# Kernel optimization log

Measured on AMD Instinct MI355X. Metric: run time of the kernel, lower is better.

Reference implementation:

```python
import jax, jax.numpy as jnp
import numpy as np
from functools import partial

K = 10
ALPHA = 0.1
N_NODES = 100000
N_EDGES = 1600000
IN_C, HID_C, OUT_C = 512, 256, 64


def setup_inputs() -> dict:
    key = jax.random.key(0)
    k1, k2, k3, k4, k5 = jax.random.split(key, 5)
    x = jax.random.normal(k1, (N_NODES, IN_C), dtype=jnp.float32)
    edge_index = jax.random.randint(k2, (2, N_EDGES), 0, N_NODES, dtype=jnp.int64)
    # Linear params (torch Linear: y = x @ W.T + b), Kaiming-ish scale
    w1 = jax.random.normal(k3, (HID_C, IN_C), dtype=jnp.float32) / np.sqrt(IN_C)
    b1 = jnp.zeros((HID_C,), dtype=jnp.float32)
    w2 = jax.random.normal(k4, (OUT_C, HID_C), dtype=jnp.float32) / np.sqrt(HID_C)
    b2 = jnp.zeros((OUT_C,), dtype=jnp.float32)
    return {"x": x, "edge_index": edge_index, "w1": w1, "b1": b1, "w2": w2, "b2": b2}


def _gcn_norm(edge_index, num_nodes):
    # add self-loops, symmetric normalization: norm_e = d[src]^-1/2 * d[dst]^-1/2
    loops = jnp.arange(num_nodes, dtype=edge_index.dtype)
    src = jnp.concatenate([edge_index[0], loops])
    dst = jnp.concatenate([edge_index[1], loops])
    ones = jnp.ones_like(dst, dtype=jnp.float32)
    deg = jax.ops.segment_sum(ones, dst, num_segments=num_nodes)
    dinv = jnp.where(deg > 0, jax.lax.rsqrt(deg), 0.0)
    norm = dinv[src] * dinv[dst]
    return src, dst, norm


def reference(x, edge_index, w1, b1, w2, b2):
    # inference mode: dropout = identity
    h = jax.nn.relu(x @ w1.T + b1)
    h = h @ w2.T + b2  # [N, OUT_C]
    n = x.shape[0]
    src, dst, norm = _gcn_norm(edge_index, n)
    h0 = h

    def step(hcur, _):
        msg = hcur[src] * norm[:, None]                      # gather [E+N, C]
        agg = jax.ops.segment_sum(msg, dst, num_segments=n)  # scatter-add [N, C]
        return (1.0 - ALPHA) * agg + ALPHA * h0, None

    h, _ = jax.lax.scan(step, h, None, length=K)
    return h
```

## Files before the change

### kernel.cpp

```cpp
#include <hip/hip_runtime.h>
#include <hip/hip_bf16.h>

#define N_NODES 100000
#define N_EDGES 1600000
#define IN_C 512
#define HID_C 256
#define OUT_C 64
#define K_ITERS 10
#define ALPHA 0.1f

typedef float f32x4 __attribute__((ext_vector_type(4)));
typedef _Float16 f16;
typedef _Float16 f16x4 __attribute__((ext_vector_type(4)));
typedef _Float16 f16x8 __attribute__((ext_vector_type(8)));

#define MFMA16(a, b, c) __builtin_amdgcn_mfma_f32_16x16x32_f16((a), (b), (c), 0, 0, 0)

__device__ __forceinline__ void gload16(const void* g, void* l) {
    __builtin_amdgcn_global_load_lds(
        (const __attribute__((address_space(1))) unsigned int*)g,
        (__attribute__((address_space(3))) unsigned int*)l, 16, 0, 0);
}

__global__ void k_count(const int* __restrict__ ei, int* __restrict__ cnt, int E) {
    int e = blockIdx.x * blockDim.x + threadIdx.x;
    if (e < E) atomicAdd(&cnt[ei[E + e]], 1);
}

__global__ void k_dinv(const int* __restrict__ cnt, float* __restrict__ dinv, int n) {
    int i = blockIdx.x * blockDim.x + threadIdx.x;
    if (i < n) dinv[i] = rsqrtf((float)cnt[i] + 1.0f);
}

#define SCB 1024
__global__ __launch_bounds__(256) void k_scan1(const int* __restrict__ cnt,
                                               int* __restrict__ bsum, int n) {
    __shared__ int s[256];
    int b = blockIdx.x, t = threadIdx.x;
    int base = b * SCB + t * 4;
    int local = 0;
#pragma unroll
    for (int j = 0; j < 4; ++j) {
        int i = base + j;
        if (i < n) local += cnt[i];
    }
    s[t] = local;
    __syncthreads();
    for (int off = 1; off < 256; off <<= 1) {
        int u = (t >= off) ? s[t - off] : 0;
        __syncthreads();
        s[t] += u;
        __syncthreads();
    }
    if (t == 255) bsum[b] = s[255];
}

__global__ __launch_bounds__(128) void k_scan2(const int* __restrict__ bsum,
                                               int* __restrict__ boff, int G,
                                               int* __restrict__ row_ptr, int n, int total) {
    __shared__ int s[128];
    int t = threadIdx.x;
    int v = (t < G) ? bsum[t] : 0;
    s[t] = v;
    __syncthreads();
    for (int off = 1; off < 128; off <<= 1) {
        int u = (t >= off) ? s[t - off] : 0;
        __syncthreads();
        s[t] += u;
        __syncthreads();
    }
    if (t < G) boff[t] = s[t] - v;
    if (t == 0) row_ptr[n] = total;
}

__global__ __launch_bounds__(256) void k_scan3(const int* __restrict__ cnt,
                                               const int* __restrict__ boff,
                                               int* __restrict__ row_ptr,
                                               int* __restrict__ cursor, int n) {
    __shared__ int s[256];
    int b = blockIdx.x, t = threadIdx.x;
    int base = b * SCB + t * 4;
    int c4[4];
    int local = 0;
#pragma unroll
    for (int j = 0; j < 4; ++j) {
        int i = base + j;
        c4[j] = (i < n) ? cnt[i] : 0;
        local += c4[j];
    }
    s[t] = local;
    __syncthreads();
    for (int off = 1; off < 256; off <<= 1) {
        int u = (t >= off) ? s[t - off] : 0;
        __syncthreads();
        s[t] += u;
        __syncthreads();
    }
    int run = boff[b] + s[t] - local;
#pragma unroll
    for (int j = 0; j < 4; ++j) {
        int i = base + j;
        if (i < n) {
            row_ptr[i] = run;
            cursor[i] = run;
            run += c4[j];
        }
    }
}

__global__ void k_fill(const int* __restrict__ ei, const float* __restrict__ dinv,
                       int* __restrict__ cursor, int2* __restrict__ csr_pack, int E) {
    int e = blockIdx.x * blockDim.x + threadIdx.x;
    if (e < E) {
        int s = ei[e];
        int d = ei[E + e];
        int pos = atomicAdd(&cursor[d], 1);
        csr_pack[pos] = make_int2(s, __float_as_int(dinv[s] * dinv[d]));
    }
}

__global__ void k_cast(const float* __restrict__ in, f16* __restrict__ out, int n) {
    int i = blockIdx.x * blockDim.x + threadIdx.x;
    if (i < n) out[i] = (f16)in[i];
}

__global__ __launch_bounds__(256, 4) void k_mlp2(
    const float* __restrict__ x,
    const f16* __restrict__ w1h,
    const float* __restrict__ b1,
    const f16* __restrict__ w2h,
    const float* __restrict__ b2,
    f16* __restrict__ h016, f16* __restrict__ hcur16, int n) {
    __shared__ __align__(16) union {
        struct {
            f16 Ah[64 * 40];
            f16 Bh[256 * 32];
        } p1;
        struct {
            f16 Hh[64 * 264];
        } p2;
    } sm;

    const int tid = threadIdx.x;
    const int l = tid & 63;
    const int w = tid >> 6;
    const int lr = l & 15;
    const int kg = l >> 4;
    const int row0 = blockIdx.x * 64;

    f32x4 acc[4][4];
#pragma unroll
    for (int m = 0; m < 4; ++m)
#pragma unroll
        for (int nf = 0; nf < 4; ++nf) acc[m][nf] = (f32x4)0.0f;

    for (int k0 = 0; k0 < IN_C; k0 += 32) {
#pragma unroll
        for (int i = 0; i < 4; ++i) {
            int slot = tid + 256 * i;
            int row = slot >> 2;
            int kc = (slot & 3) ^ ((row >> 1) & 3);
            size_t goff = (size_t)row * IN_C + k0 + kc * 8;
            int sbase = (w * 64 + 256 * i) * 8;
            gload16(w1h + goff, &sm.p1.Bh[sbase]);
        }
#pragma unroll
        for (int i = 0; i < 2; ++i) {
            int f4 = tid + 256 * i;
            int r = f4 >> 3, kk = (f4 & 7) * 4;
            int gr = row0 + r;
            if (gr >= n) gr = n - 1;
            float4 v = *(const float4*)&x[(size_t)gr * IN_C + k0 + kk];
            f16x4 h4;
            h4.x = (f16)v.x;
            h4.y = (f16)v.y;
            h4.z = (f16)v.z;
            h4.w = (f16)v.w;
            *(f16x4*)&sm.p1.Ah[r * 40 + kk] = h4;
        }
        __syncthreads();

        f16x8 ah[4], bh[4];
#pragma unroll
        for (int m = 0; m < 4; ++m)
            ah[m] = *(const f16x8*)&sm.p1.Ah[(m * 16 + lr) * 40 + kg * 8];
#pragma unroll
        for (int nf = 0; nf < 4; ++nf) {
            int row = w * 64 + nf * 16 + lr;
            int kc = kg ^ ((row >> 1) & 3);
            bh[nf] = *(const f16x8*)&sm.p1.Bh[row * 32 + kc * 8];
        }
#pragma unroll
        for (int m = 0; m < 4; ++m)
#pragma unroll
            for (int nf = 0; nf < 4; ++nf)
                acc[m][nf] = MFMA16(ah[m], bh[nf], acc[m][nf]);
        __syncthreads();
    }

#pragma unroll
    for (int m = 0; m < 4; ++m)
#pragma unroll
        for (int nf = 0; nf < 4; ++nf) {
            int col = w * 64 + nf * 16 + lr;
            float bb = b1[col];
#pragma unroll
            for (int r = 0; r < 4; ++r) {
                int row = m * 16 + kg * 4 + r;
                float hv = acc[m][nf][r] + bb;
                hv = fmaxf(hv, 0.0f);
                sm.p2.Hh[row * 264 + col] = (f16)hv;
            }
        }
    __syncthreads();

    f32x4 acc2[4];
#pragma unroll
    for (int m = 0; m < 4; ++m) acc2[m] = (f32x4)0.0f;
    const int col2 = w * 16 + lr;

#pragma unroll
    for (int k0 = 0; k0 < HID_C; k0 += 32) {
        f16x8 b2h = *(const f16x8*)&w2h[(size_t)col2 * HID_C + k0 + kg * 8];
#pragma unroll
        for (int m = 0; m < 4; ++m) {
            f16x8 a2h = *(const f16x8*)&sm.p2.Hh[(m * 16 + lr) * 264 + k0 + kg * 8];
            acc2[m] = MFMA16(a2h, b2h, acc2[m]);
        }
    }

    float bb2 = b2[col2];
#pragma unroll
    for (int m = 0; m < 4; ++m)
#pragma unroll
        for (int r = 0; r < 4; ++r) {
            int grow = row0 + m * 16 + kg * 4 + r;
            if (grow < n) {
                float vv = acc2[m][r] + bb2;
                size_t idx = (size_t)grow * OUT_C + col2;
                h016[idx] = (f16)vv;
                hcur16[idx] = (f16)vv;
            }
        }
}

__global__ __launch_bounds__(256) void k_prop16(const f16* __restrict__ hin,
                                                const f16* __restrict__ h016,
                                                f16* __restrict__ hout,
                                                float* __restrict__ dout,
                                                const int* __restrict__ row_ptr,
                                                const int2* __restrict__ csr_pack,
                                                const float* __restrict__ dinv,
                                                int n, int final_iter) {
    const int gwave = (blockIdx.x * blockDim.x + threadIdx.x) >> 6;
    const int lane = threadIdx.x & 63;
    const int g = lane >> 3;
    const int cl = lane & 7;

    int node_raw = gwave * 8 + g;
    bool node_valid = node_raw < n;
    int node = node_valid ? node_raw : (n - 1);

    int e0 = row_ptr[node], e1 = row_ptr[node + 1];
    int nb = (e1 - e0 + 7) >> 3;
    nb = max(nb, __shfl_xor(nb, 8));
    nb = max(nb, __shfl_xor(nb, 16));
    nb = max(nb, __shfl_xor(nb, 32));

    float a[8];
#pragma unroll
    for (int q = 0; q < 8; ++q) a[q] = 0.0f;
    const int gbase = g * 8;

    for (int b = 0; b < nb; ++b) {
        int mbase = e0 + b * 8;
        int midx = min(mbase + cl, N_EDGES - 1);
        int2 meta = csr_pack[midx];
#pragma unroll
        for (int j = 0; j < 8; ++j) {
            int s = __shfl(meta.x, gbase + j);
            float wv = __int_as_float(__shfl(meta.y, gbase + j));
            if (mbase + j < e1) {
                f16x8 v = *(const f16x8*)&hin[(size_t)s * OUT_C + cl * 8];
#pragma unroll
                for (int q = 0; q < 8; ++q) a[q] += wv * (float)v[q];
            }
        }
    }

    float dv = dinv[node];
    float d2 = dv * dv;
    size_t idx = (size_t)node * OUT_C + cl * 8;
    f16x8 sv = *(const f16x8*)&hin[idx];
    f16x8 h0v = *(const f16x8*)&h016[idx];
    float r[8];
#pragma unroll
    for (int q = 0; q < 8; ++q)
        r[q] = (1.0f - ALPHA) * (a[q] + d2 * (float)sv[q]) + ALPHA * (float)h0v[q];

    if (node_valid) {
        f16x8 o;
#pragma unroll
        for (int q = 0; q < 8; ++q) o[q] = (f16)r[q];
        *(f16x8*)&hout[idx] = o;
        if (final_iter) {
            float4 o0 = make_float4(r[0], r[1], r[2], r[3]);
            float4 o1 = make_float4(r[4], r[5], r[6], r[7]);
            *(float4*)&dout[idx] = o0;
            *(float4*)&dout[idx + 4] = o1;
        }
    }
}

extern "C" void kernel_launch(void* const* d_in, const int* in_sizes, int n_in,
                              void* d_out, int out_size, void* d_ws, size_t ws_size,
                              hipStream_t stream) {
    const float* x  = (const float*)d_in[0];
    const int*   ei = (const int*)d_in[1];
    const float* w1 = (const float*)d_in[2];
    const float* b1 = (const float*)d_in[3];
    const float* w2 = (const float*)d_in[4];
    const float* b2 = (const float*)d_in[5];
    float* dout = (float*)d_out;

    const int N = N_NODES;
    const int E = N_EDGES;
    const int G = (N + SCB - 1) / SCB;

    f16*   h16A    = (f16*)d_ws;
    f16*   h16B    = h16A + (size_t)N * OUT_C;
    f16*   h016    = h16B + (size_t)N * OUT_C;
    int2*  csr_pack = (int2*)(h016 + (size_t)N * OUT_C);
    float* dinv    = (float*)(csr_pack + E);
    int*   cnt     = (int*)(dinv + N);
    int*   row_ptr = cnt + N;
    int*   cursor  = row_ptr + (N + 1);
    f16*   w1h     = (f16*)(cursor + N);
    f16*   w2h     = w1h + (size_t)HID_C * IN_C;
    int*   bsum    = (int*)(w2h + (size_t)OUT_C * HID_C);
    int*   boff    = bsum + 128;

    hipMemsetAsync(cnt, 0, (size_t)N * sizeof(int), stream);

    k_count<<<(E + 255) / 256, 256, 0, stream>>>(ei, cnt, E);
    k_dinv<<<(N + 255) / 256, 256, 0, stream>>>(cnt, dinv, N);
    k_scan1<<<G, 256, 0, stream>>>(cnt, bsum, N);
    k_scan2<<<1, 128, 0, stream>>>(bsum, boff, G, row_ptr, N, E);
    k_scan3<<<G, 256, 0, stream>>>(cnt, boff, row_ptr, cursor, N);
    k_fill<<<(E + 255) / 256, 256, 0, stream>>>(ei, dinv, cursor, csr_pack, E);

    k_cast<<<(HID_C * IN_C + 255) / 256, 256, 0, stream>>>(w1, w1h, HID_C * IN_C);
    k_cast<<<(OUT_C * HID_C + 255) / 256, 256, 0, stream>>>(w2, w2h, OUT_C * HID_C);

    k_mlp2<<<(N + 63) / 64, 256, 0, stream>>>(x, w1h, b1, w2h, b2, h016, h16A, N);

    const int pwaves = (N + 7) / 8;
    const int pblocks = (pwaves * 64 + 255) / 256;
    for (int it = 0; it < K_ITERS; ++it) {
        const f16* pin = (it & 1) ? h16B : h16A;
        f16* pout = (it & 1) ? h16A : h16B;
        k_prop16<<<pblocks, 256, 0, stream>>>(pin, h016, pout, dout, row_ptr,
                                              csr_pack, dinv, N,
                                              it == K_ITERS - 1 ? 1 : 0);
    }
}
```

Before: 637.8 us.

## Bucket nodes by degree for balanced propagation waves; prefetch x rows in MLP

Adds a degree histogram, a scan and a permutation pass so each propagation wave processes nodes of similar in-degree, which cuts the idle lanes from the per-wave max-degree loop bound. The permutation is computed once and reused across all propagation iterations. Separately, the first MLP stage now loads the next x tile into registers before the MMA work on the current tile, to hide global load latency. The cost is three extra small kernels, an indirect perm lookup per node, and scattered output writes from permuted nodes.

```diff
diff --git a/kernel.cpp b/kernel.cpp
--- a/kernel.cpp
+++ b/kernel.cpp
@@ -116,6 +116,37 @@
         int d = ei[E + e];
         int pos = atomicAdd(&cursor[d], 1);
         csr_pack[pos] = make_int2(s, __float_as_int(dinv[s] * dinv[d]));
+    }
+}
+
+__global__ void k_hist(const int* __restrict__ cnt, int* __restrict__ hist, int n) {
+    int i = blockIdx.x * blockDim.x + threadIdx.x;
+    if (i < n) atomicAdd(&hist[min(cnt[i], 255)], 1);
+}
+
+__global__ __launch_bounds__(256) void k_hscan(const int* __restrict__ hist,
+                                               int* __restrict__ hcur) {
+    __shared__ int s[256];
+    int t = threadIdx.x;
+    int v = hist[t];
+    s[t] = v;
+    __syncthreads();
+    for (int off = 1; off < 256; off <<= 1) {
+        int u = (t >= off) ? s[t - off] : 0;
+        __syncthreads();
+        s[t] += u;
+        __syncthreads();
+    }
+    hcur[t] = s[t] - v;
+}
+
+__global__ void k_perm(const int* __restrict__ cnt, int* __restrict__ hcur,
+                       int* __restrict__ perm, int n) {
+    int i = blockIdx.x * blockDim.x + threadIdx.x;
+    if (i < n) {
+        int b = min(cnt[i], 255);
+        int pos = atomicAdd(&hcur[b], 1);
+        perm[pos] = i;
     }
 }
 
@@ -148,13 +179,24 @@
     const int kg = l >> 4;
     const int row0 = blockIdx.x * 64;
 
+    const int r0 = tid >> 3, kk0 = (tid & 7) * 4;
+    const int r1 = (tid + 256) >> 3, kk1 = (tid & 7) * 4;
+    int gr0 = row0 + r0; if (gr0 >= n) gr0 = n - 1;
+    int gr1 = row0 + r1; if (gr1 >= n) gr1 = n - 1;
+    const float* xp0 = &x[(size_t)gr0 * IN_C + kk0];
+    const float* xp1 = &x[(size_t)gr1 * IN_C + kk1];
+
     f32x4 acc[4][4];
 #pragma unroll
     for (int m = 0; m < 4; ++m)
 #pragma unroll
         for (int nf = 0; nf < 4; ++nf) acc[m][nf] = (f32x4)0.0f;
 
-    for (int k0 = 0; k0 < IN_C; k0 += 32) {
+    float4 xv0 = *(const float4*)xp0;
+    float4 xv1 = *(const float4*)xp1;
+
+    for (int ks = 0; ks < 16; ++ks) {
+        const int k0 = ks * 32;
 #pragma unroll
         for (int i = 0; i < 4; ++i) {
             int slot = tid + 256 * i;
@@ -164,21 +206,19 @@
             int sbase = (w * 64 + 256 * i) * 8;
             gload16(w1h + goff, &sm.p1.Bh[sbase]);
         }
-#pragma unroll
-        for (int i = 0; i < 2; ++i) {
-            int f4 = tid + 256 * i;
-            int r = f4 >> 3, kk = (f4 & 7) * 4;
-            int gr = row0 + r;
-            if (gr >= n) gr = n - 1;
-            float4 v = *(const float4*)&x[(size_t)gr * IN_C + k0 + kk];
+        {
             f16x4 h4;
-            h4.x = (f16)v.x;
-            h4.y = (f16)v.y;
-            h4.z = (f16)v.z;
-            h4.w = (f16)v.w;
-            *(f16x4*)&sm.p1.Ah[r * 40 + kk] = h4;
-        }
-        __syncthreads();
+            h4.x = (f16)xv0.x; h4.y = (f16)xv0.y; h4.z = (f16)xv0.z; h4.w = (f16)xv0.w;
+            *(f16x4*)&sm.p1.Ah[r0 * 40 + kk0] = h4;
+            h4.x = (f16)xv1.x; h4.y = (f16)xv1.y; h4.z = (f16)xv1.z; h4.w = (f16)xv1.w;
+            *(f16x4*)&sm.p1.Ah[r1 * 40 + kk1] = h4;
+        }
+        __syncthreads();
+
+        if (ks < 15) {
+            xv0 = *(const float4*)(xp0 + k0 + 32);
+            xv1 = *(const float4*)(xp1 + k0 + 32);
+        }
 
         f16x8 ah[4], bh[4];
 #pragma unroll
@@ -251,15 +291,16 @@
                                                 const int* __restrict__ row_ptr,
                                                 const int2* __restrict__ csr_pack,
                                                 const float* __restrict__ dinv,
+                                                const int* __restrict__ perm,
                                                 int n, int final_iter) {
     const int gwave = (blockIdx.x * blockDim.x + threadIdx.x) >> 6;
     const int lane = threadIdx.x & 63;
     const int g = lane >> 3;
     const int cl = lane & 7;
 
-    int node_raw = gwave * 8 + g;
-    bool node_valid = node_raw < n;
-    int node = node_valid ? node_raw : (n - 1);
+    int sp = gwave * 8 + g;
+    bool node_valid = sp < n;
+    int node = perm[node_valid ? sp : (n - 1)];
 
     int e0 = row_ptr[node], e1 = row_ptr[node + 1];
     int nb = (e1 - e0 + 7) >> 3;
@@ -335,12 +376,16 @@
     int*   cnt     = (int*)(dinv + N);
     int*   row_ptr = cnt + N;
     int*   cursor  = row_ptr + (N + 1);
-    f16*   w1h     = (f16*)(cursor + N);
+    int*   perm    = cursor + N;
+    f16*   w1h     = (f16*)(perm + N);
     f16*   w2h     = w1h + (size_t)HID_C * IN_C;
     int*   bsum    = (int*)(w2h + (size_t)OUT_C * HID_C);
     int*   boff    = bsum + 128;
+    int*   hist    = boff + 128;
+    int*   hcur    = hist + 256;
 
     hipMemsetAsync(cnt, 0, (size_t)N * sizeof(int), stream);
+    hipMemsetAsync(hist, 0, 256 * sizeof(int), stream);
 
     k_count<<<(E + 255) / 256, 256, 0, stream>>>(ei, cnt, E);
     k_dinv<<<(N + 255) / 256, 256, 0, stream>>>(cnt, dinv, N);
@@ -349,6 +394,10 @@
     k_scan3<<<G, 256, 0, stream>>>(cnt, boff, row_ptr, cursor, N);
     k_fill<<<(E + 255) / 256, 256, 0, stream>>>(ei, dinv, cursor, csr_pack, E);
 
+    k_hist<<<(N + 255) / 256, 256, 0, stream>>>(cnt, hist, N);
+    k_hscan<<<1, 256, 0, stream>>>(hist, hcur);
+    k_perm<<<(N + 255) / 256, 256, 0, stream>>>(cnt, hcur, perm, N);
+
     k_cast<<<(HID_C * IN_C + 255) / 256, 256, 0, stream>>>(w1, w1h, HID_C * IN_C);
     k_cast<<<(OUT_C * HID_C + 255) / 256, 256, 0, stream>>>(w2, w2h, OUT_C * HID_C);
 
@@ -360,7 +409,7 @@
         const f16* pin = (it & 1) ? h16B : h16A;
         f16* pout = (it & 1) ? h16A : h16B;
         k_prop16<<<pblocks, 256, 0, stream>>>(pin, h016, pout, dout, row_ptr,
-                                              csr_pack, dinv, N,
+                                              csr_pack, dinv, perm, N,
                                               it == K_ITERS - 1 ? 1 : 0);
     }
 }
```

Result: slower. 1.222 ms (+91.6%).
